# Optimization experiments

Hardware: AMD Instinct MI355X
Metric: run time of the kernel (lower is better)

Reference implementation:

```python
import jax, jax.numpy as jnp
import numpy as np

B, M, F, E = 64, 1024, 4, 256      # batch, memory length, tokens-per-memory-cell, emb_size
NW, HOPS, PL = 32000, 3, 128       # vocab, hops, profile_len


def _embed(table, idx):
    # nn.Embedding with padding_idx=0 -> index 0 maps to zero vector
    return table[idx] * (idx != 0)[..., None].astype(table.dtype)


def _gru_step(x, h, Wih, Whh, bih, bhh):
    # single-step PyTorch GRU cell
    gi = x @ Wih.T + bih
    gh = h @ Whh.T + bhh
    ir, iz, i_n = jnp.split(gi, 3, axis=-1)
    hr, hz, h_n = jnp.split(gh, 3, axis=-1)
    r = jax.nn.sigmoid(ir + hr)
    z = jax.nn.sigmoid(iz + hz)
    n = jnp.tanh(i_n + r * h_n)
    return (1.0 - z) * n + z * h


def setup_inputs() -> dict:
    key = jax.random.key(0)
    ks = jax.random.split(key, 13)
    # HOPS+1 unique embedding tables: A[0..hops-1] plus C[hops-1]; C[h]=tables[h+1] (weight tying)
    tables = (jax.random.normal(ks[0], (HOPS + 1, NW, E)) * 0.1).at[:, 0, :].set(0.0)
    s = 1.0 / np.sqrt(E)
    Wih = jax.random.uniform(ks[1], (3 * E, E), minval=-s, maxval=s)
    Whh = jax.random.uniform(ks[2], (3 * E, E), minval=-s, maxval=s)
    bih = jax.random.uniform(ks[3], (3 * E,), minval=-s, maxval=s)
    bhh = jax.random.uniform(ks[4], (3 * E,), minval=-s, maxval=s)
    sp = 1.0 / np.sqrt(PL)
    Wp = jax.random.uniform(ks[5], (E, PL), minval=-sp, maxval=sp)
    bp = jax.random.uniform(ks[6], (E,), minval=-sp, maxval=sp)
    sv = 1.0 / np.sqrt(2 * E)
    Wv = jax.random.uniform(ks[7], (NW, 2 * E), minval=-sv, maxval=sv)
    bv = jax.random.uniform(ks[8], (NW,), minval=-sv, maxval=sv)
    context = jax.random.randint(ks[9], (B, M, F), 0, NW)
    y_ = jax.random.randint(ks[10], (B,), 0, NW)
    h_ = jax.random.normal(ks[11], (1, B, E))
    profile_encoding = jax.random.normal(ks[12], (B, PL))
    return dict(tables=tables, Wih=Wih, Whh=Whh, bih=bih, bhh=bhh, Wp=Wp, bp=bp,
                Wv=Wv, bv=bv, context=context, y_=y_, h_=h_,
                profile_encoding=profile_encoding)


def reference(tables, Wih, Whh, bih, bhh, Wp, bp, Wv, bv, context, y_, h_, profile_encoding):
    # load_memory (eval mode: no word dropout): memories[h] = sum over F of table[h] embeddings
    ctx = context.reshape(B, M * F)
    mems = [_embed(tables[hop], ctx).reshape(B, M, F, E).sum(axis=2) for hop in range(HOPS + 1)]
    # decoder step
    m = _embed(tables[1], y_)                    # C[0](y_)
    h = _gru_step(m, h_[0], Wih, Whh, bih, bhh)  # [B, E]
    q = h
    p = p_vocab = p_resto = None
    for hop in range(HOPS):
        p_ = mems[hop] * q[:, None, :]           # [B, M, E] elementwise attention scores
        p = p_.sum(axis=2)                        # [B, M]
        attn = jax.nn.softmax(p, axis=1)
        o = jnp.einsum('bm,bme->be', attn, mems[hop + 1])
        if hop == 0:
            p_vocab = jnp.concatenate([h, o], axis=1) @ Wv.T + bv  # uses q[0]=h
        if hop == 1:
            enc = profile_encoding @ Wp.T + bp   # [B, E]
            p_resto = jnp.einsum('bme,be->bm', p_, enc)
        q = q + o
    return p, p_vocab, p_resto, h[None]          # p_ptr, p_vocab, p_resto, h [1,B,E]
```

## Files before the change

### kernel.cpp

```cpp
#include <hip/hip_runtime.h>
#include <cstdint>

#define B_ 64
#define M_ 1024
#define F_ 4
#define E_ 256
#define NW_ 32000
#define PL_ 128

#define P_OFF   0
#define PV_OFF  65536
#define PR_OFF  2113536
#define H_OFF   2179072

typedef unsigned short u16;
typedef unsigned int u32;

typedef __bf16 bf16x8 __attribute__((ext_vector_type(8)));
typedef float f32x4 __attribute__((ext_vector_type(4)));

__device__ __forceinline__ u16 f2bf(float f) {
    u32 x = __builtin_bit_cast(u32, f);
    u32 r = (x + 0x7fffu + ((x >> 16) & 1u)) >> 16;
    return (u16)r;
}
__device__ __forceinline__ float bflo(u32 v) {
    return __builtin_bit_cast(float, v << 16);
}
__device__ __forceinline__ float bfhi(u32 v) {
    return __builtin_bit_cast(float, v & 0xffff0000u);
}
__device__ __forceinline__ float dot8(uint4 u, float4 qa, float4 qb) {
    return bflo(u.x) * qa.x + bfhi(u.x) * qa.y + bflo(u.y) * qa.z + bfhi(u.y) * qa.w +
           bflo(u.z) * qb.x + bfhi(u.z) * qb.y + bflo(u.w) * qb.z + bfhi(u.w) * qb.w;
}
__device__ __forceinline__ void acc8(uint4 u, float* a) {
    a[0] += bflo(u.x); a[1] += bfhi(u.x); a[2] += bflo(u.y); a[3] += bfhi(u.y);
    a[4] += bflo(u.z); a[5] += bfhi(u.z); a[6] += bflo(u.w); a[7] += bfhi(u.w);
}
__device__ __forceinline__ uint4 pack8(const float* s) {
    uint4 u;
    u.x = (u32)f2bf(s[0]) | ((u32)f2bf(s[1]) << 16);
    u.y = (u32)f2bf(s[2]) | ((u32)f2bf(s[3]) << 16);
    u.z = (u32)f2bf(s[4]) | ((u32)f2bf(s[5]) << 16);
    u.w = (u32)f2bf(s[6]) | ((u32)f2bf(s[7]) << 16);
    return u;
}
__device__ __forceinline__ bf16x8 pack_bf8(float4 a, float4 b) {
    union { u16 s[8]; bf16x8 v; } u;
    u.s[0] = f2bf(a.x); u.s[1] = f2bf(a.y); u.s[2] = f2bf(a.z); u.s[3] = f2bf(a.w);
    u.s[4] = f2bf(b.x); u.s[5] = f2bf(b.y); u.s[6] = f2bf(b.z); u.s[7] = f2bf(b.w);
    return u.v;
}

__global__ __launch_bounds__(256) void k_conv(
    const float* __restrict__ tables, u16* __restrict__ t0b, u16* __restrict__ t12)
{
    int t = blockIdx.y;
    int c = blockIdx.x * 256 + threadIdx.x;
    const float* src = tables + (size_t)t * NW_ * E_ + (size_t)c * 8;
    float4 a = *(const float4*)src;
    float4 b = *(const float4*)(src + 4);
    float s[8] = {a.x, a.y, a.z, a.w, b.x, b.y, b.z, b.w};
    uint4 u = pack8(s);
    if (t == 0) {
        *(uint4*)(t0b + (size_t)c * 8) = u;
    } else {
        int row = c >> 5, e = (c & 31) * 8;
        *(uint4*)(t12 + (size_t)row * 512 + (t - 1) * 256 + e) = u;
    }
}

__global__ __launch_bounds__(256) void k_gru(
    const float* __restrict__ tables, const float* __restrict__ Wih,
    const float* __restrict__ Whh, const float* __restrict__ bih,
    const float* __restrict__ bhh, const float* __restrict__ Wp,
    const float* __restrict__ bp, const int* __restrict__ y,
    const float* __restrict__ h_, const float* __restrict__ pe,
    float* __restrict__ q0, float* __restrict__ enc, float* __restrict__ outh)
{
    int b = blockIdx.x, t = threadIdx.x;
    __shared__ float m_s[E_], h_s[E_], pe_s[PL_];
    int yb = y[b];
    m_s[t] = tables[(size_t)NW_ * E_ + (size_t)yb * E_ + t];
    h_s[t] = h_[b * E_ + t];
    if (t < PL_) pe_s[t] = pe[b * PL_ + t];
    __syncthreads();

    float g_i[3], g_h[3];
#pragma unroll
    for (int g = 0; g < 3; g++) {
        int j = g * E_ + t;
        float ai = bih[j], ah = bhh[j];
        const float4* wi = (const float4*)(Wih + (size_t)j * E_);
        const float4* wh = (const float4*)(Whh + (size_t)j * E_);
#pragma unroll 8
        for (int e = 0; e < E_ / 4; e++) {
            float4 a = wi[e], c = wh[e];
            ai += a.x * m_s[4 * e] + a.y * m_s[4 * e + 1] +
                  a.z * m_s[4 * e + 2] + a.w * m_s[4 * e + 3];
            ah += c.x * h_s[4 * e] + c.y * h_s[4 * e + 1] +
                  c.z * h_s[4 * e + 2] + c.w * h_s[4 * e + 3];
        }
        g_i[g] = ai; g_h[g] = ah;
    }
    float r = 1.f / (1.f + expf(-(g_i[0] + g_h[0])));
    float z = 1.f / (1.f + expf(-(g_i[1] + g_h[1])));
    float n = tanhf(g_i[2] + r * g_h[2]);
    float hv = (1.f - z) * n + z * h_s[t];
    q0[b * E_ + t] = hv;
    outh[b * E_ + t] = hv;

    float ea = bp[t];
    const float4* wp = (const float4*)(Wp + (size_t)t * PL_);
#pragma unroll 8
    for (int p = 0; p < PL_ / 4; p++) {
        float4 a = wp[p];
        ea += a.x * pe_s[4 * p] + a.y * pe_s[4 * p + 1] +
              a.z * pe_s[4 * p + 2] + a.w * pe_s[4 * p + 3];
    }
    enc[b * E_ + t] = ea;
}

__global__ __launch_bounds__(256) void k_scores0(
    const u16* __restrict__ t0b, const int* __restrict__ ctx,
    const float* __restrict__ q, float* __restrict__ p_ws)
{
    int b = blockIdx.y, grp = blockIdx.x;
    int lane = threadIdx.x & 63, w = threadIdx.x >> 6;
    int h = lane >> 5, l32 = lane & 31, e0 = l32 * 8;
    float4 qa = *(const float4*)(q + b * E_ + e0);
    float4 qb = *(const float4*)(q + b * E_ + e0 + 4);
    int mbase = grp * 32 + w * 8;
    const int4* cp = (const int4*)(ctx + ((size_t)b * M_ + mbase) * 4);
    int4 c[8];
#pragma unroll
    for (int i = 0; i < 8; i++) c[i] = cp[i];

    float pa[8];
#pragma unroll
    for (int i = 0; i < 8; i++) {
        int ia = h ? c[i].y : c[i].x;
        int ib = h ? c[i].w : c[i].z;
        uint4 ra = *(const uint4*)(t0b + (size_t)ia * E_ + e0);
        uint4 rb = *(const uint4*)(t0b + (size_t)ib * E_ + e0);
        pa[i] = dot8(ra, qa, qb) + dot8(rb, qa, qb);
    }
#pragma unroll
    for (int o = 32; o > 0; o >>= 1)
#pragma unroll
        for (int i = 0; i < 8; i++) pa[i] += __shfl_xor(pa[i], o, 64);
    if (lane == 0)
#pragma unroll
        for (int i = 0; i < 8; i++) p_ws[(size_t)b * M_ + mbase + i] = pa[i];
}

__global__ __launch_bounds__(256) void k_soft(
    float* __restrict__ p_ws, const float* __restrict__ qcur,
    float* __restrict__ qnext)
{
    int b = blockIdx.x, t = threadIdx.x;
    __shared__ float red[256];
    float4 v = *(const float4*)(p_ws + (size_t)b * M_ + t * 4);
    float lm = fmaxf(fmaxf(v.x, v.y), fmaxf(v.z, v.w));
    red[t] = lm;
    __syncthreads();
    for (int s = 128; s > 0; s >>= 1) {
        if (t < s) red[t] = fmaxf(red[t], red[t + s]);
        __syncthreads();
    }
    float mx = red[0];
    __syncthreads();
    float e0 = expf(v.x - mx), e1 = expf(v.y - mx);
    float e2 = expf(v.z - mx), e3 = expf(v.w - mx);
    red[t] = e0 + e1 + e2 + e3;
    __syncthreads();
    for (int s = 128; s > 0; s >>= 1) {
        if (t < s) red[t] += red[t + s];
        __syncthreads();
    }
    float inv = 1.f / red[0];
    float4 o = make_float4(e0 * inv, e1 * inv, e2 * inv, e3 * inv);
    *(float4*)(p_ws + (size_t)b * M_ + t * 4) = o;
    qnext[b * E_ + t] = qcur[b * E_ + t];
}

__global__ __launch_bounds__(256) void k_mems12(
    const u16* __restrict__ t12, const int* __restrict__ ctx,
    const float* __restrict__ attn0, u16* __restrict__ mems1,
    u16* __restrict__ mems2, float* __restrict__ q1)
{
    int b = blockIdx.y, grp = blockIdx.x;
    int lane = threadIdx.x & 63, w = threadIdx.x >> 6;
    int h = lane >> 5, l32 = lane & 31, e0 = l32 * 8;
    int mbase = grp * 32 + w * 8;
    const int4* cp = (const int4*)(ctx + ((size_t)b * M_ + mbase) * 4);
    int4 c[8];
#pragma unroll
    for (int i = 0; i < 8; i++) c[i] = cp[i];
    float4 a01 = *(const float4*)(attn0 + (size_t)b * M_ + mbase);
    float4 a23 = *(const float4*)(attn0 + (size_t)b * M_ + mbase + 4);
    float wg[8] = {a01.x, a01.y, a01.z, a01.w, a23.x, a23.y, a23.z, a23.w};

    u16* mout = h ? mems2 : mems1;
    float o_acc[8] = {0, 0, 0, 0, 0, 0, 0, 0};
#pragma unroll
    for (int i = 0; i < 8; i++) {
        size_t off = (size_t)h * 256 + e0;
        uint4 r0 = *(const uint4*)(t12 + (size_t)c[i].x * 512 + off);
        uint4 r1 = *(const uint4*)(t12 + (size_t)c[i].y * 512 + off);
        uint4 r2 = *(const uint4*)(t12 + (size_t)c[i].z * 512 + off);
        uint4 r3 = *(const uint4*)(t12 + (size_t)c[i].w * 512 + off);
        float acc[8] = {0, 0, 0, 0, 0, 0, 0, 0};
        acc8(r0, acc); acc8(r1, acc); acc8(r2, acc); acc8(r3, acc);
        *(uint4*)(mout + ((size_t)(b * M_ + mbase + i)) * 256 + e0) = pack8(acc);
        if (h == 0) {
            float wgt = wg[i];
#pragma unroll
            for (int j = 0; j < 8; j++) o_acc[j] += wgt * acc[j];
        }
    }
    __shared__ float red[4][E_];
    if (h == 0)
#pragma unroll
        for (int j = 0; j < 8; j++) red[w][e0 + j] = o_acc[j];
    __syncthreads();
    int t = threadIdx.x;
    float s = red[0][t] + red[1][t] + red[2][t] + red[3][t];
    atomicAdd(q1 + b * E_ + t, s);
}

template <int MODE>
__global__ __launch_bounds__(256) void k_sscores(
    const u16* __restrict__ mems, const float* __restrict__ q,
    const float* __restrict__ enc, float* __restrict__ p_ws,
    float* __restrict__ out)
{
    int b = blockIdx.y, grp = blockIdx.x;
    int lane = threadIdx.x & 63, w = threadIdx.x >> 6;
    int h = lane >> 5, l32 = lane & 31, e0 = l32 * 8;
    float4 qa = *(const float4*)(q + b * E_ + e0);
    float4 qb = *(const float4*)(q + b * E_ + e0 + 4);
    float4 ea4 = make_float4(0, 0, 0, 0), eb4 = make_float4(0, 0, 0, 0);
    if (MODE == 1) {
        float4 ev = *(const float4*)(enc + b * E_ + e0);
        float4 ew = *(const float4*)(enc + b * E_ + e0 + 4);
        ea4 = make_float4(qa.x * ev.x, qa.y * ev.y, qa.z * ev.z, qa.w * ev.w);
        eb4 = make_float4(qb.x * ew.x, qb.y * ew.y, qb.z * ew.z, qb.w * ew.w);
    }
    int mbase = grp * 32 + w * 8;
    float pa[4], pr[4];
#pragma unroll
    for (int i = 0; i < 4; i++) {
        int m = mbase + 2 * i + h;
        uint4 r = *(const uint4*)(mems + ((size_t)(b * M_ + m)) * 256 + e0);
        pa[i] = dot8(r, qa, qb);
        if (MODE == 1) pr[i] = dot8(r, ea4, eb4);
    }
#pragma unroll
    for (int o = 16; o > 0; o >>= 1)
#pragma unroll
        for (int i = 0; i < 4; i++) {
            pa[i] += __shfl_xor(pa[i], o, 64);
            if (MODE == 1) pr[i] += __shfl_xor(pr[i], o, 64);
        }
    if (l32 == 0) {
#pragma unroll
        for (int i = 0; i < 4; i++) {
            int m = mbase + 2 * i + h;
            if (MODE == 2) out[P_OFF + (size_t)b * M_ + m] = pa[i];
            else           p_ws[(size_t)b * M_ + m] = pa[i];
            if (MODE == 1) out[PR_OFF + (size_t)b * M_ + m] = pr[i];
        }
    }
}

__global__ __launch_bounds__(256) void k_so(
    const u16* __restrict__ mems, const float* __restrict__ attn,
    float* __restrict__ qnext)
{
    int b = blockIdx.y, ch = blockIdx.x;
    int lane = threadIdx.x & 63, w = threadIdx.x >> 6;
    int h = lane >> 5, l32 = lane & 31, e0 = l32 * 8;
    int m0 = ch * 128;
    float acc[8] = {0, 0, 0, 0, 0, 0, 0, 0};
    for (int i = 0; i < 16; i++) {
        int m = m0 + i * 8 + w * 2 + h;
        float wgt = attn[(size_t)b * M_ + m];
        uint4 r = *(const uint4*)(mems + ((size_t)(b * M_ + m)) * 256 + e0);
        acc[0] += wgt * bflo(r.x); acc[1] += wgt * bfhi(r.x);
        acc[2] += wgt * bflo(r.y); acc[3] += wgt * bfhi(r.y);
        acc[4] += wgt * bflo(r.z); acc[5] += wgt * bfhi(r.z);
        acc[6] += wgt * bflo(r.w); acc[7] += wgt * bfhi(r.w);
    }
    __shared__ float red[8][E_];
    int hw = threadIdx.x >> 5;
#pragma unroll
    for (int j = 0; j < 8; j++) red[hw][e0 + j] = acc[j];
    __syncthreads();
    int t = threadIdx.x;
    float s = 0.f;
#pragma unroll
    for (int k = 0; k < 8; k++) s += red[k][t];
    atomicAdd(qnext + b * E_ + t, s);
}

__global__ __launch_bounds__(256) void k_pvocab(
    const float* __restrict__ Wv, const float* __restrict__ bv,
    const float* __restrict__ q0, const float* __restrict__ q1,
    float* __restrict__ out)
{
    __shared__ u16 X[64 * 512];
    int t = threadIdx.x;
#pragma unroll
    for (int it = 0; it < 16; it++) {
        int id = t + it * 256;
        int bb = id >> 6, c = id & 63;
        float v[8];
        if (c < 32) {
            const float* s = q0 + bb * E_ + c * 8;
#pragma unroll
            for (int j = 0; j < 8; j++) v[j] = s[j];
        } else {
            const float* s1 = q1 + bb * E_ + (c - 32) * 8;
            const float* s0 = q0 + bb * E_ + (c - 32) * 8;
#pragma unroll
            for (int j = 0; j < 8; j++) v[j] = s1[j] - s0[j];
        }
        uint4 uv = pack8(v);
        *(uint4*)(&X[bb * 512 + ((c ^ (bb & 7)) << 3)]) = uv;
    }
    __syncthreads();

    int lane = t & 63, w = t >> 6;
    int n0 = blockIdx.x * 128 + w * 32;
    int l15 = lane & 15, quad = lane >> 4;
    f32x4 acc[4][2];
#pragma unroll
    for (int mt = 0; mt < 4; mt++)
#pragma unroll
        for (int nt = 0; nt < 2; nt++)
            acc[mt][nt] = f32x4{0.f, 0.f, 0.f, 0.f};

    for (int ks = 0; ks < 16; ks++) {
        bf16x8 a[4], bfr[2];
#pragma unroll
        for (int mt = 0; mt < 4; mt++) {
            int m = mt * 16 + l15;
            int c = ks * 4 + quad;
            a[mt] = *(const bf16x8*)(&X[m * 512 + ((c ^ (m & 7)) << 3)]);
        }
#pragma unroll
        for (int nt = 0; nt < 2; nt++) {
            int n = n0 + nt * 16 + l15;
            const float4* wp = (const float4*)(Wv + (size_t)n * 512 + ks * 32 + quad * 8);
            bfr[nt] = pack_bf8(wp[0], wp[1]);
        }
#pragma unroll
        for (int mt = 0; mt < 4; mt++)
#pragma unroll
            for (int nt = 0; nt < 2; nt++)
                acc[mt][nt] = __builtin_amdgcn_mfma_f32_16x16x32_bf16(
                    a[mt], bfr[nt], acc[mt][nt], 0, 0, 0);
    }
#pragma unroll
    for (int nt = 0; nt < 2; nt++) {
        int n = n0 + nt * 16 + l15;
        float bvv = bv[n];
#pragma unroll
        for (int mt = 0; mt < 4; mt++) {
#pragma unroll
            for (int j = 0; j < 4; j++) {
                int m = mt * 16 + quad * 4 + j;
                out[PV_OFF + (size_t)m * 32000 + n] = acc[mt][nt][j] + bvv;
            }
        }
    }
}

extern "C" void kernel_launch(void* const* d_in, const int* in_sizes, int n_in,
                              void* d_out, int out_size, void* d_ws, size_t ws_size,
                              hipStream_t stream)
{
    const float* tables = (const float*)d_in[0];
    const float* Wih = (const float*)d_in[1];
    const float* Whh = (const float*)d_in[2];
    const float* bih = (const float*)d_in[3];
    const float* bhh = (const float*)d_in[4];
    const float* Wp  = (const float*)d_in[5];
    const float* bp  = (const float*)d_in[6];
    const float* Wv  = (const float*)d_in[7];
    const float* bv  = (const float*)d_in[8];
    const int* ctx = (const int*)d_in[9];
    const int* y   = (const int*)d_in[10];
    const float* h_  = (const float*)d_in[11];
    const float* pe  = (const float*)d_in[12];
    float* out = (float*)d_out;

    float* Wf   = (float*)d_ws;
    float* q    = Wf;
    float* enc  = Wf + 65536;
    float* p_ws = Wf + 81920;
    char* base  = (char*)d_ws + 589824;
    u16* t0b    = (u16*)base;
    u16* t12    = (u16*)(base + 16384000);
    u16* mems1  = (u16*)(base + 16384000 + 32768000);
    u16* mems2  = (u16*)(base + 16384000 + 32768000 + 33554432);

    k_conv<<<dim3(4000, 3), 256, 0, stream>>>(tables, t0b, t12);
    k_gru<<<64, 256, 0, stream>>>(tables, Wih, Whh, bih, bhh, Wp, bp, y, h_, pe,
                                  q, enc, out + H_OFF);
    k_scores0<<<dim3(32, 64), 256, 0, stream>>>(t0b, ctx, q, p_ws);
    k_soft<<<64, 256, 0, stream>>>(p_ws, q, q + 16384);
    k_mems12<<<dim3(32, 64), 256, 0, stream>>>(t12, ctx, p_ws, mems1, mems2,
                                               q + 16384);
    k_sscores<1><<<dim3(32, 64), 256, 0, stream>>>(mems1, q + 16384, enc, p_ws, out);
    k_soft<<<64, 256, 0, stream>>>(p_ws, q + 16384, q + 32768);
    k_so<<<dim3(8, 64), 256, 0, stream>>>(mems2, p_ws, q + 32768);
    k_sscores<2><<<dim3(32, 64), 256, 0, stream>>>(mems2, q + 32768, enc, p_ws, out);
    k_pvocab<<<250, 256, 0, stream>>>(Wv, bv, q, q + 16384, out);
}
```

Before: 399.5 us.

## Replace memory materialization with vocab-wide score GEMMs and gathered sums

Instead of building bf16 copies of the tables and materializing summed memory cells, the pipeline first computes query-vs-vocabulary scores for every table row with MFMA GEMMs, using a hi/lo bf16 split of the query to keep precision. Per-memory scores are then gathered as sums of four vocab scores, and the attention-weighted outputs are accumulated directly from fp32 table rows. This removes the full-table conversion pass and the large mems1/mems2 writes and reads. In exchange it scores all 32000 words per batch row and adds several small kernels and extra workspace for the score matrices.

```diff
diff --git a/kernel.cpp b/kernel.cpp
--- a/kernel.cpp
+++ b/kernel.cpp
@@ -24,19 +24,8 @@
     u32 r = (x + 0x7fffu + ((x >> 16) & 1u)) >> 16;
     return (u16)r;
 }
-__device__ __forceinline__ float bflo(u32 v) {
-    return __builtin_bit_cast(float, v << 16);
-}
-__device__ __forceinline__ float bfhi(u32 v) {
-    return __builtin_bit_cast(float, v & 0xffff0000u);
-}
-__device__ __forceinline__ float dot8(uint4 u, float4 qa, float4 qb) {
-    return bflo(u.x) * qa.x + bfhi(u.x) * qa.y + bflo(u.y) * qa.z + bfhi(u.y) * qa.w +
-           bflo(u.z) * qb.x + bfhi(u.z) * qb.y + bflo(u.w) * qb.z + bfhi(u.w) * qb.w;
-}
-__device__ __forceinline__ void acc8(uint4 u, float* a) {
-    a[0] += bflo(u.x); a[1] += bfhi(u.x); a[2] += bflo(u.y); a[3] += bfhi(u.y);
-    a[4] += bflo(u.z); a[5] += bfhi(u.z); a[6] += bflo(u.w); a[7] += bfhi(u.w);
+__device__ __forceinline__ float bf2f(u16 h) {
+    return __builtin_bit_cast(float, (u32)h << 16);
 }
 __device__ __forceinline__ uint4 pack8(const float* s) {
     uint4 u;
@@ -53,31 +42,14 @@
     return u.v;
 }
 
-__global__ __launch_bounds__(256) void k_conv(
-    const float* __restrict__ tables, u16* __restrict__ t0b, u16* __restrict__ t12)
-{
-    int t = blockIdx.y;
-    int c = blockIdx.x * 256 + threadIdx.x;
-    const float* src = tables + (size_t)t * NW_ * E_ + (size_t)c * 8;
-    float4 a = *(const float4*)src;
-    float4 b = *(const float4*)(src + 4);
-    float s[8] = {a.x, a.y, a.z, a.w, b.x, b.y, b.z, b.w};
-    uint4 u = pack8(s);
-    if (t == 0) {
-        *(uint4*)(t0b + (size_t)c * 8) = u;
-    } else {
-        int row = c >> 5, e = (c & 31) * 8;
-        *(uint4*)(t12 + (size_t)row * 512 + (t - 1) * 256 + e) = u;
-    }
-}
-
 __global__ __launch_bounds__(256) void k_gru(
     const float* __restrict__ tables, const float* __restrict__ Wih,
     const float* __restrict__ Whh, const float* __restrict__ bih,
     const float* __restrict__ bhh, const float* __restrict__ Wp,
     const float* __restrict__ bp, const int* __restrict__ y,
     const float* __restrict__ h_, const float* __restrict__ pe,
-    float* __restrict__ q0, float* __restrict__ enc, float* __restrict__ outh)
+    float* __restrict__ q0, float* __restrict__ q1, float* __restrict__ q2,
+    float* __restrict__ enc, float* __restrict__ outh, u16* __restrict__ Qc0)
 {
     int b = blockIdx.x, t = threadIdx.x;
     __shared__ float m_s[E_], h_s[E_], pe_s[PL_];
@@ -109,7 +81,12 @@
     float n = tanhf(g_i[2] + r * g_h[2]);
     float hv = (1.f - z) * n + z * h_s[t];
     q0[b * E_ + t] = hv;
+    q1[b * E_ + t] = hv;
+    q2[b * E_ + t] = hv;
     outh[b * E_ + t] = hv;
+    u16 hi = f2bf(hv);
+    Qc0[(size_t)b * E_ + t] = hi;
+    Qc0[(size_t)(B_ + b) * E_ + t] = f2bf(hv - bf2f(hi));
 
     float ea = bp[t];
     const float4* wp = (const float4*)(Wp + (size_t)t * PL_);
@@ -122,47 +99,98 @@
     enc[b * E_ + t] = ea;
 }
 
-__global__ __launch_bounds__(256) void k_scores0(
-    const u16* __restrict__ t0b, const int* __restrict__ ctx,
-    const float* __restrict__ q, float* __restrict__ p_ws)
-{
-    int b = blockIdx.y, grp = blockIdx.x;
-    int lane = threadIdx.x & 63, w = threadIdx.x >> 6;
-    int h = lane >> 5, l32 = lane & 31, e0 = l32 * 8;
-    float4 qa = *(const float4*)(q + b * E_ + e0);
-    float4 qb = *(const float4*)(q + b * E_ + e0 + 4);
-    int mbase = grp * 32 + w * 8;
-    const int4* cp = (const int4*)(ctx + ((size_t)b * M_ + mbase) * 4);
-    int4 c[8];
-#pragma unroll
-    for (int i = 0; i < 8; i++) c[i] = cp[i];
-
-    float pa[8];
-#pragma unroll
-    for (int i = 0; i < 8; i++) {
-        int ia = h ? c[i].y : c[i].x;
-        int ib = h ? c[i].w : c[i].z;
-        uint4 ra = *(const uint4*)(t0b + (size_t)ia * E_ + e0);
-        uint4 rb = *(const uint4*)(t0b + (size_t)ib * E_ + e0);
-        pa[i] = dot8(ra, qa, qb) + dot8(rb, qa, qb);
-    }
-#pragma unroll
-    for (int o = 32; o > 0; o >>= 1)
-#pragma unroll
-        for (int i = 0; i < 8; i++) pa[i] += __shfl_xor(pa[i], o, 64);
-    if (lane == 0)
-#pragma unroll
-        for (int i = 0; i < 8; i++) p_ws[(size_t)b * M_ + mbase + i] = pa[i];
-}
-
-__global__ __launch_bounds__(256) void k_soft(
-    float* __restrict__ p_ws, const float* __restrict__ qcur,
-    float* __restrict__ qnext)
+template <int WE>
+__global__ __launch_bounds__(256) void k_qprep(
+    const float* __restrict__ qsrc, const float* __restrict__ enc,
+    u16* __restrict__ Qc)
 {
     int b = blockIdx.x, t = threadIdx.x;
+    float v = qsrc[b * E_ + t];
+    u16 hi = f2bf(v);
+    Qc[(size_t)b * E_ + t] = hi;
+    Qc[(size_t)(B_ + b) * E_ + t] = f2bf(v - bf2f(hi));
+    if (WE) {
+        float e = v * enc[b * E_ + t];
+        u16 h2 = f2bf(e);
+        Qc[(size_t)(2 * B_ + b) * E_ + t] = h2;
+        Qc[(size_t)(3 * B_ + b) * E_ + t] = f2bf(e - bf2f(h2));
+    }
+}
+
+template <int NQ>
+__global__ __launch_bounds__(256) void k_sgemm(
+    const float* __restrict__ T, const u16* __restrict__ Qc,
+    float* __restrict__ OA, float* __restrict__ OB)
+{
+    constexpr int NT = NQ * 4;
+    __shared__ float lds[64][65];
+    int t = threadIdx.x, lane = t & 63, wv = t >> 6;
+    int l15 = lane & 15, quad = lane >> 4;
+    int w0 = blockIdx.x * 64;
+    const float* arow = T + (size_t)(w0 + wv * 16 + l15) * E_;
+    f32x4 acc[NT];
+#pragma unroll
+    for (int nt = 0; nt < NT; nt++) acc[nt] = f32x4{0.f, 0.f, 0.f, 0.f};
+#pragma unroll
+    for (int ks = 0; ks < 8; ks++) {
+        int k0 = ks * 32 + quad * 8;
+        float4 a0 = *(const float4*)(arow + k0);
+        float4 a1 = *(const float4*)(arow + k0 + 4);
+        bf16x8 af = pack_bf8(a0, a1);
+#pragma unroll
+        for (int nt = 0; nt < NT; nt++) {
+            bf16x8 bfr = *(const bf16x8*)(Qc + (size_t)(nt * 16 + l15) * E_ + k0);
+            acc[nt] = __builtin_amdgcn_mfma_f32_16x16x32_bf16(af, bfr, acc[nt], 0, 0, 0);
+        }
+    }
+#pragma unroll
+    for (int arr = 0; arr < NQ / 2; arr++) {
+        float* O = arr ? OB : OA;
+        if (arr) __syncthreads();
+#pragma unroll
+        for (int nt = 0; nt < 4; nt++)
+#pragma unroll
+            for (int j = 0; j < 4; j++)
+                lds[wv * 16 + quad * 4 + j][nt * 16 + l15] =
+                    acc[arr * 8 + nt][j] + acc[arr * 8 + nt + 4][j];
+        __syncthreads();
+        int bb = t >> 2, ws = (t & 3) * 16;
+        float vv[16];
+#pragma unroll
+        for (int i = 0; i < 16; i++) vv[i] = lds[ws + i][bb];
+        float* orow = O + (size_t)bb * NW_ + w0 + ws;
+        *(float4*)(orow)      = make_float4(vv[0], vv[1], vv[2], vv[3]);
+        *(float4*)(orow + 4)  = make_float4(vv[4], vv[5], vv[6], vv[7]);
+        *(float4*)(orow + 8)  = make_float4(vv[8], vv[9], vv[10], vv[11]);
+        *(float4*)(orow + 12) = make_float4(vv[12], vv[13], vv[14], vv[15]);
+    }
+}
+
+template <int MODE>
+__global__ __launch_bounds__(256) void k_gsm(
+    const float* __restrict__ S, const float* __restrict__ SR,
+    const int* __restrict__ ctx, float* __restrict__ attn,
+    float* __restrict__ outpr)
+{
+    int b = blockIdx.x, t = threadIdx.x;
+    const float* Sb = S + (size_t)b * NW_;
+    const int4* cp = (const int4*)(ctx + ((size_t)b * M_ + t * 4) * F_);
+    int4 c0 = cp[0], c1 = cp[1], c2 = cp[2], c3 = cp[3];
+    float p0 = Sb[c0.x] + Sb[c0.y] + Sb[c0.z] + Sb[c0.w];
+    float p1 = Sb[c1.x] + Sb[c1.y] + Sb[c1.z] + Sb[c1.w];
+    float p2 = Sb[c2.x] + Sb[c2.y] + Sb[c2.z] + Sb[c2.w];
+    float p3 = Sb[c3.x] + Sb[c3.y] + Sb[c3.z] + Sb[c3.w];
+    if constexpr (MODE == 1) {
+        const float* Rb = SR + (size_t)b * NW_;
+        float r0 = Rb[c0.x] + Rb[c0.y] + Rb[c0.z] + Rb[c0.w];
+        float r1 = Rb[c1.x] + Rb[c1.y] + Rb[c1.z] + Rb[c1.w];
+        float r2 = Rb[c2.x] + Rb[c2.y] + Rb[c2.z] + Rb[c2.w];
+        float r3 = Rb[c3.x] + Rb[c3.y] + Rb[c3.z] + Rb[c3.w];
+        *(float4*)(outpr + PR_OFF + (size_t)b * M_ + t * 4) =
+            make_float4(r0, r1, r2, r3);
+    }
     __shared__ float red[256];
-    float4 v = *(const float4*)(p_ws + (size_t)b * M_ + t * 4);
-    float lm = fmaxf(fmaxf(v.x, v.y), fmaxf(v.z, v.w));
+    float lm = fmaxf(fmaxf(p0, p1), fmaxf(p2, p3));
     red[t] = lm;
     __syncthreads();
     for (int s = 128; s > 0; s >>= 1) {
@@ -171,8 +199,8 @@
     }
     float mx = red[0];
     __syncthreads();
-    float e0 = expf(v.x - mx), e1 = expf(v.y - mx);
-    float e2 = expf(v.z - mx), e3 = expf(v.w - mx);
+    float e0 = expf(p0 - mx), e1 = expf(p1 - mx);
+    float e2 = expf(p2 - mx), e3 = expf(p3 - mx);
     red[t] = e0 + e1 + e2 + e3;
     __syncthreads();
     for (int s = 128; s > 0; s >>= 1) {
@@ -180,129 +208,43 @@
         __syncthreads();
     }
     float inv = 1.f / red[0];
-    float4 o = make_float4(e0 * inv, e1 * inv, e2 * inv, e3 * inv);
-    *(float4*)(p_ws + (size_t)b * M_ + t * 4) = o;
-    qnext[b * E_ + t] = qcur[b * E_ + t];
-}
-
-__global__ __launch_bounds__(256) void k_mems12(
-    const u16* __restrict__ t12, const int* __restrict__ ctx,
-    const float* __restrict__ attn0, u16* __restrict__ mems1,
-    u16* __restrict__ mems2, float* __restrict__ q1)
-{
-    int b = blockIdx.y, grp = blockIdx.x;
-    int lane = threadIdx.x & 63, w = threadIdx.x >> 6;
-    int h = lane >> 5, l32 = lane & 31, e0 = l32 * 8;
-    int mbase = grp * 32 + w * 8;
-    const int4* cp = (const int4*)(ctx + ((size_t)b * M_ + mbase) * 4);
-    int4 c[8];
-#pragma unroll
-    for (int i = 0; i < 8; i++) c[i] = cp[i];
-    float4 a01 = *(const float4*)(attn0 + (size_t)b * M_ + mbase);
-    float4 a23 = *(const float4*)(attn0 + (size_t)b * M_ + mbase + 4);
-    float wg[8] = {a01.x, a01.y, a01.z, a01.w, a23.x, a23.y, a23.z, a23.w};
-
-    u16* mout = h ? mems2 : mems1;
-    float o_acc[8] = {0, 0, 0, 0, 0, 0, 0, 0};
-#pragma unroll
-    for (int i = 0; i < 8; i++) {
-        size_t off = (size_t)h * 256 + e0;
-        uint4 r0 = *(const uint4*)(t12 + (size_t)c[i].x * 512 + off);
-        uint4 r1 = *(const uint4*)(t12 + (size_t)c[i].y * 512 + off);
-        uint4 r2 = *(const uint4*)(t12 + (size_t)c[i].z * 512 + off);
-        uint4 r3 = *(const uint4*)(t12 + (size_t)c[i].w * 512 + off);
-        float acc[8] = {0, 0, 0, 0, 0, 0, 0, 0};
-        acc8(r0, acc); acc8(r1, acc); acc8(r2, acc); acc8(r3, acc);
-        *(uint4*)(mout + ((size_t)(b * M_ + mbase + i)) * 256 + e0) = pack8(acc);
-        if (h == 0) {
-            float wgt = wg[i];
-#pragma unroll
-            for (int j = 0; j < 8; j++) o_acc[j] += wgt * acc[j];
-        }
-    }
-    __shared__ float red[4][E_];
-    if (h == 0)
-#pragma unroll
-        for (int j = 0; j < 8; j++) red[w][e0 + j] = o_acc[j];
-    __syncthreads();
-    int t = threadIdx.x;
-    float s = red[0][t] + red[1][t] + red[2][t] + red[3][t];
-    atomicAdd(q1 + b * E_ + t, s);
-}
-
-template <int MODE>
-__global__ __launch_bounds__(256) void k_sscores(
-    const u16* __restrict__ mems, const float* __restrict__ q,
-    const float* __restrict__ enc, float* __restrict__ p_ws,
+    *(float4*)(attn + (size_t)b * M_ + t * 4) =
+        make_float4(e0 * inv, e1 * inv, e2 * inv, e3 * inv);
+}
+
+__global__ __launch_bounds__(256) void k_g2(
+    const float* __restrict__ S, const int* __restrict__ ctx,
     float* __restrict__ out)
 {
-    int b = blockIdx.y, grp = blockIdx.x;
-    int lane = threadIdx.x & 63, w = threadIdx.x >> 6;
-    int h = lane >> 5, l32 = lane & 31, e0 = l32 * 8;
-    float4 qa = *(const float4*)(q + b * E_ + e0);
-    float4 qb = *(const float4*)(q + b * E_ + e0 + 4);
-    float4 ea4 = make_float4(0, 0, 0, 0), eb4 = make_float4(0, 0, 0, 0);
-    if (MODE == 1) {
-        float4 ev = *(const float4*)(enc + b * E_ + e0);
-        float4 ew = *(const float4*)(enc + b * E_ + e0 + 4);
-        ea4 = make_float4(qa.x * ev.x, qa.y * ev.y, qa.z * ev.z, qa.w * ev.w);
-        eb4 = make_float4(qb.x * ew.x, qb.y * ew.y, qb.z * ew.z, qb.w * ew.w);
-    }
-    int mbase = grp * 32 + w * 8;
-    float pa[4], pr[4];
-#pragma unroll
-    for (int i = 0; i < 4; i++) {
-        int m = mbase + 2 * i + h;
-        uint4 r = *(const uint4*)(mems + ((size_t)(b * M_ + m)) * 256 + e0);
-        pa[i] = dot8(r, qa, qb);
-        if (MODE == 1) pr[i] = dot8(r, ea4, eb4);
-    }
-#pragma unroll
-    for (int o = 16; o > 0; o >>= 1)
-#pragma unroll
-        for (int i = 0; i < 4; i++) {
-            pa[i] += __shfl_xor(pa[i], o, 64);
-            if (MODE == 1) pr[i] += __shfl_xor(pr[i], o, 64);
-        }
-    if (l32 == 0) {
-#pragma unroll
-        for (int i = 0; i < 4; i++) {
-            int m = mbase + 2 * i + h;
-            if (MODE == 2) out[P_OFF + (size_t)b * M_ + m] = pa[i];
-            else           p_ws[(size_t)b * M_ + m] = pa[i];
-            if (MODE == 1) out[PR_OFF + (size_t)b * M_ + m] = pr[i];
-        }
-    }
-}
-
-__global__ __launch_bounds__(256) void k_so(
-    const u16* __restrict__ mems, const float* __restrict__ attn,
-    float* __restrict__ qnext)
-{
-    int b = blockIdx.y, ch = blockIdx.x;
-    int lane = threadIdx.x & 63, w = threadIdx.x >> 6;
-    int h = lane >> 5, l32 = lane & 31, e0 = l32 * 8;
-    int m0 = ch * 128;
-    float acc[8] = {0, 0, 0, 0, 0, 0, 0, 0};
-    for (int i = 0; i < 16; i++) {
-        int m = m0 + i * 8 + w * 2 + h;
-        float wgt = attn[(size_t)b * M_ + m];
-        uint4 r = *(const uint4*)(mems + ((size_t)(b * M_ + m)) * 256 + e0);
-        acc[0] += wgt * bflo(r.x); acc[1] += wgt * bfhi(r.x);
-        acc[2] += wgt * bflo(r.y); acc[3] += wgt * bfhi(r.y);
-        acc[4] += wgt * bflo(r.z); acc[5] += wgt * bfhi(r.z);
-        acc[6] += wgt * bflo(r.w); acc[7] += wgt * bfhi(r.w);
-    }
-    __shared__ float red[8][E_];
-    int hw = threadIdx.x >> 5;
-#pragma unroll
-    for (int j = 0; j < 8; j++) red[hw][e0 + j] = acc[j];
-    __syncthreads();
-    int t = threadIdx.x;
-    float s = 0.f;
-#pragma unroll
-    for (int k = 0; k < 8; k++) s += red[k][t];
-    atomicAdd(qnext + b * E_ + t, s);
+    int b = blockIdx.y;
+    int m = blockIdx.x * 256 + threadIdx.x;
+    const float* Sb = S + (size_t)b * NW_;
+    int4 c = *(const int4*)(ctx + ((size_t)b * M_ + m) * F_);
+    out[P_OFF + (size_t)b * M_ + m] = Sb[c.x] + Sb[c.y] + Sb[c.z] + Sb[c.w];
+}
+
+template <int NADD>
+__global__ __launch_bounds__(256) void k_oacc(
+    const float* __restrict__ T, const int* __restrict__ ctx,
+    const float* __restrict__ attn, float* __restrict__ qa,
+    float* __restrict__ qb)
+{
+    int b = blockIdx.y, chv = blockIdx.x, t = threadIdx.x;
+    int m0 = chv * 128;
+    __shared__ int cidx[512];
+    __shared__ float aw[128];
+    if (t < 128) aw[t] = attn[(size_t)b * M_ + m0 + t];
+    ((int2*)cidx)[t] = ((const int2*)(ctx + ((size_t)b * M_ + m0) * F_))[t];
+    __syncthreads();
+    float acc0 = 0.f, acc1 = 0.f;
+#pragma unroll 8
+    for (int r = 0; r < 512; r += 2) {
+        acc0 += aw[r >> 2]       * T[(size_t)cidx[r] * E_ + t];
+        acc1 += aw[(r + 1) >> 2] * T[(size_t)cidx[r + 1] * E_ + t];
+    }
+    float acc = acc0 + acc1;
+    atomicAdd(qa + b * E_ + t, acc);
+    if constexpr (NADD == 2) atomicAdd(qb + b * E_ + t, acc);
 }
 
 __global__ __launch_bounds__(256) void k_pvocab(
@@ -398,25 +340,33 @@
     float* out = (float*)d_out;
 
     float* Wf   = (float*)d_ws;
-    float* q    = Wf;
-    float* enc  = Wf + 65536;
-    float* p_ws = Wf + 81920;
-    char* base  = (char*)d_ws + 589824;
-    u16* t0b    = (u16*)base;
-    u16* t12    = (u16*)(base + 16384000);
-    u16* mems1  = (u16*)(base + 16384000 + 32768000);
-    u16* mems2  = (u16*)(base + 16384000 + 32768000 + 33554432);
-
-    k_conv<<<dim3(4000, 3), 256, 0, stream>>>(tables, t0b, t12);
+    float* q0v  = Wf;
+    float* q1v  = Wf + 16384;
+    float* q2v  = Wf + 32768;
+    float* encv = Wf + 49152;
+    float* attn = Wf + 65536;
+    u16* Qc0 = (u16*)(Wf + 131072);
+    u16* Qc1 = Qc0 + 32768;
+    u16* Qc2 = Qc1 + 65536;
+    float* S0 = (float*)(Qc2 + 32768);
+    float* S1 = S0 + (size_t)B_ * NW_;
+    float* SRb = S1 + (size_t)B_ * NW_;
+    float* S2 = SRb + (size_t)B_ * NW_;
+    const float* T0 = tables;
+    const float* T1 = tables + (size_t)NW_ * E_;
+    const float* T2 = tables + 2 * (size_t)NW_ * E_;
+
     k_gru<<<64, 256, 0, stream>>>(tables, Wih, Whh, bih, bhh, Wp, bp, y, h_, pe,
-                                  q, enc, out + H_OFF);
-    k_scores0<<<dim3(32, 64), 256, 0, stream>>>(t0b, ctx, q, p_ws);
-    k_soft<<<64, 256, 0, stream>>>(p_ws, q, q + 16384);
-    k_mems12<<<dim3(32, 64), 256, 0, stream>>>(t12, ctx, p_ws, mems1, mems2,
-                                               q + 16384);
-    k_sscores<1><<<dim3(32, 64), 256, 0, stream>>>(mems1, q + 16384, enc, p_ws, out);
-    k_soft<<<64, 256, 0, stream>>>(p_ws, q + 16384, q + 32768);
-    k_so<<<dim3(8, 64), 256, 0, stream>>>(mems2, p_ws, q + 32768);
-    k_sscores<2><<<dim3(32, 64), 256, 0, stream>>>(mems2, q + 32768, enc, p_ws, out);
-    k_pvocab<<<250, 256, 0, stream>>>(Wv, bv, q, q + 16384, out);
-}
+                                  q0v, q1v, q2v, encv, out + H_OFF, Qc0);
+    k_sgemm<2><<<500, 256, 0, stream>>>(T0, Qc0, S0, nullptr);
+    k_gsm<0><<<64, 256, 0, stream>>>(S0, nullptr, ctx, attn, nullptr);
+    k_oacc<2><<<dim3(8, 64), 256, 0, stream>>>(T1, ctx, attn, q1v, q2v);
+    k_qprep<1><<<64, 256, 0, stream>>>(q1v, encv, Qc1);
+    k_sgemm<4><<<500, 256, 0, stream>>>(T1, Qc1, S1, SRb);
+    k_gsm<1><<<64, 256, 0, stream>>>(S1, SRb, ctx, attn, out);
+    k_oacc<1><<<dim3(8, 64), 256, 0, stream>>>(T2, ctx, attn, q2v, nullptr);
+    k_qprep<0><<<64, 256, 0, stream>>>(q2v, nullptr, Qc2);
+    k_sgemm<2><<<500, 256, 0, stream>>>(T2, Qc2, S2, nullptr);
+    k_g2<<<dim3(4, 64), 256, 0, stream>>>(S2, ctx, out);
+    k_pvocab<<<250, 256, 0, stream>>>(Wv, bv, q0v, q1v, out);
+}
```

Result: slower. 461.0 us (+15.4%).

## Fuse all phases into one persistent cooperative kernel with grid syncs

Applied to the files above, without the earlier changes.

Replaces the ten separate kernel launches with a single cooperative persistent kernel that runs each stage as a phase separated by grid-wide barriers, using a shared-memory union. The GRU runs on dedicated blocks while the table conversion runs on the rest, and the final score phase is overlapped with the vocab projection in the same loop. The vocab GEMM is retiled to 64 columns per block with batched weight loads. This removes launch gaps and inter-kernel idle time, at the cost of grid-sync overhead, limited grid size (at most 512 blocks), and lower per-phase occupancy.

```diff
diff --git a/kernel.cpp b/kernel.cpp
--- a/kernel.cpp
+++ b/kernel.cpp
@@ -1,5 +1,8 @@
 #include <hip/hip_runtime.h>
+#include <hip/hip_cooperative_groups.h>
 #include <cstdint>
+
+namespace cg = cooperative_groups;
 
 #define B_ 64
 #define M_ 1024
@@ -53,11 +56,19 @@
     return u.v;
 }
 
-__global__ __launch_bounds__(256) void k_conv(
+union SharedU {
+    struct { float m_s[E_]; float h_s[E_]; float pe_s[PL_]; } gru;
+    float red1[256];
+    float red4[4][E_];
+    float red8[8][E_];
+    u16 X[64 * 512];
+};
+
+__device__ __forceinline__ void ph_conv(int vb, int tid,
     const float* __restrict__ tables, u16* __restrict__ t0b, u16* __restrict__ t12)
 {
-    int t = blockIdx.y;
-    int c = blockIdx.x * 256 + threadIdx.x;
+    int t = vb / 4000;
+    int c = (vb % 4000) * 256 + tid;
     const float* src = tables + (size_t)t * NW_ * E_ + (size_t)c * 8;
     float4 a = *(const float4*)src;
     float4 b = *(const float4*)(src + 4);
@@ -71,7 +82,7 @@
     }
 }
 
-__global__ __launch_bounds__(256) void k_gru(
+__device__ __forceinline__ void ph_gru(int b, int tid, SharedU& su,
     const float* __restrict__ tables, const float* __restrict__ Wih,
     const float* __restrict__ Whh, const float* __restrict__ bih,
     const float* __restrict__ bhh, const float* __restrict__ Wp,
@@ -79,12 +90,12 @@
     const float* __restrict__ h_, const float* __restrict__ pe,
     float* __restrict__ q0, float* __restrict__ enc, float* __restrict__ outh)
 {
-    int b = blockIdx.x, t = threadIdx.x;
-    __shared__ float m_s[E_], h_s[E_], pe_s[PL_];
+    int t = tid;
+    __syncthreads();
     int yb = y[b];
-    m_s[t] = tables[(size_t)NW_ * E_ + (size_t)yb * E_ + t];
-    h_s[t] = h_[b * E_ + t];
-    if (t < PL_) pe_s[t] = pe[b * PL_ + t];
+    su.gru.m_s[t] = tables[(size_t)NW_ * E_ + (size_t)yb * E_ + t];
+    su.gru.h_s[t] = h_[b * E_ + t];
+    if (t < PL_) su.gru.pe_s[t] = pe[b * PL_ + t];
     __syncthreads();
 
     float g_i[3], g_h[3];
@@ -97,17 +108,17 @@
 #pragma unroll 8
         for (int e = 0; e < E_ / 4; e++) {
             float4 a = wi[e], c = wh[e];
-            ai += a.x * m_s[4 * e] + a.y * m_s[4 * e + 1] +
-                  a.z * m_s[4 * e + 2] + a.w * m_s[4 * e + 3];
-            ah += c.x * h_s[4 * e] + c.y * h_s[4 * e + 1] +
-                  c.z * h_s[4 * e + 2] + c.w * h_s[4 * e + 3];
+            ai += a.x * su.gru.m_s[4 * e] + a.y * su.gru.m_s[4 * e + 1] +
+                  a.z * su.gru.m_s[4 * e + 2] + a.w * su.gru.m_s[4 * e + 3];
+            ah += c.x * su.gru.h_s[4 * e] + c.y * su.gru.h_s[4 * e + 1] +
+                  c.z * su.gru.h_s[4 * e + 2] + c.w * su.gru.h_s[4 * e + 3];
         }
         g_i[g] = ai; g_h[g] = ah;
     }
     float r = 1.f / (1.f + expf(-(g_i[0] + g_h[0])));
     float z = 1.f / (1.f + expf(-(g_i[1] + g_h[1])));
     float n = tanhf(g_i[2] + r * g_h[2]);
-    float hv = (1.f - z) * n + z * h_s[t];
+    float hv = (1.f - z) * n + z * su.gru.h_s[t];
     q0[b * E_ + t] = hv;
     outh[b * E_ + t] = hv;
 
@@ -116,18 +127,18 @@
 #pragma unroll 8
     for (int p = 0; p < PL_ / 4; p++) {
         float4 a = wp[p];
-        ea += a.x * pe_s[4 * p] + a.y * pe_s[4 * p + 1] +
-              a.z * pe_s[4 * p + 2] + a.w * pe_s[4 * p + 3];
+        ea += a.x * su.gru.pe_s[4 * p] + a.y * su.gru.pe_s[4 * p + 1] +
+              a.z * su.gru.pe_s[4 * p + 2] + a.w * su.gru.pe_s[4 * p + 3];
     }
     enc[b * E_ + t] = ea;
 }
 
-__global__ __launch_bounds__(256) void k_scores0(
+__device__ __forceinline__ void ph_scores0(int vb, int tid,
     const u16* __restrict__ t0b, const int* __restrict__ ctx,
     const float* __restrict__ q, float* __restrict__ p_ws)
 {
-    int b = blockIdx.y, grp = blockIdx.x;
-    int lane = threadIdx.x & 63, w = threadIdx.x >> 6;
+    int grp = vb & 31, b = vb >> 5;
+    int lane = tid & 63, w = tid >> 6;
     int h = lane >> 5, l32 = lane & 31, e0 = l32 * 8;
     float4 qa = *(const float4*)(q + b * E_ + e0);
     float4 qb = *(const float4*)(q + b * E_ + e0 + 4);
@@ -155,45 +166,46 @@
         for (int i = 0; i < 8; i++) p_ws[(size_t)b * M_ + mbase + i] = pa[i];
 }
 
-__global__ __launch_bounds__(256) void k_soft(
+__device__ __forceinline__ void ph_soft(int b, int tid, SharedU& su,
     float* __restrict__ p_ws, const float* __restrict__ qcur,
     float* __restrict__ qnext)
 {
-    int b = blockIdx.x, t = threadIdx.x;
-    __shared__ float red[256];
+    int t = tid;
+    __syncthreads();
     float4 v = *(const float4*)(p_ws + (size_t)b * M_ + t * 4);
     float lm = fmaxf(fmaxf(v.x, v.y), fmaxf(v.z, v.w));
-    red[t] = lm;
+    su.red1[t] = lm;
     __syncthreads();
     for (int s = 128; s > 0; s >>= 1) {
-        if (t < s) red[t] = fmaxf(red[t], red[t + s]);
+        if (t < s) su.red1[t] = fmaxf(su.red1[t], su.red1[t + s]);
         __syncthreads();
     }
-    float mx = red[0];
+    float mx = su.red1[0];
     __syncthreads();
     float e0 = expf(v.x - mx), e1 = expf(v.y - mx);
     float e2 = expf(v.z - mx), e3 = expf(v.w - mx);
-    red[t] = e0 + e1 + e2 + e3;
+    su.red1[t] = e0 + e1 + e2 + e3;
     __syncthreads();
     for (int s = 128; s > 0; s >>= 1) {
-        if (t < s) red[t] += red[t + s];
+        if (t < s) su.red1[t] += su.red1[t + s];
         __syncthreads();
     }
-    float inv = 1.f / red[0];
+    float inv = 1.f / su.red1[0];
     float4 o = make_float4(e0 * inv, e1 * inv, e2 * inv, e3 * inv);
     *(float4*)(p_ws + (size_t)b * M_ + t * 4) = o;
     qnext[b * E_ + t] = qcur[b * E_ + t];
 }
 
-__global__ __launch_bounds__(256) void k_mems12(
+__device__ __forceinline__ void ph_mems12(int vb, int tid, SharedU& su,
     const u16* __restrict__ t12, const int* __restrict__ ctx,
     const float* __restrict__ attn0, u16* __restrict__ mems1,
     u16* __restrict__ mems2, float* __restrict__ q1)
 {
-    int b = blockIdx.y, grp = blockIdx.x;
-    int lane = threadIdx.x & 63, w = threadIdx.x >> 6;
+    int grp = vb & 31, b = vb >> 5;
+    int lane = tid & 63, w = tid >> 6;
     int h = lane >> 5, l32 = lane & 31, e0 = l32 * 8;
     int mbase = grp * 32 + w * 8;
+    __syncthreads();
     const int4* cp = (const int4*)(ctx + ((size_t)b * M_ + mbase) * 4);
     int4 c[8];
 #pragma unroll
@@ -220,24 +232,23 @@
             for (int j = 0; j < 8; j++) o_acc[j] += wgt * acc[j];
         }
     }
-    __shared__ float red[4][E_];
     if (h == 0)
 #pragma unroll
-        for (int j = 0; j < 8; j++) red[w][e0 + j] = o_acc[j];
-    __syncthreads();
-    int t = threadIdx.x;
-    float s = red[0][t] + red[1][t] + red[2][t] + red[3][t];
+        for (int j = 0; j < 8; j++) su.red4[w][e0 + j] = o_acc[j];
+    __syncthreads();
+    int t = tid;
+    float s = su.red4[0][t] + su.red4[1][t] + su.red4[2][t] + su.red4[3][t];
     atomicAdd(q1 + b * E_ + t, s);
 }
 
 template <int MODE>
-__global__ __launch_bounds__(256) void k_sscores(
+__device__ __forceinline__ void ph_sscores(int vb, int tid,
     const u16* __restrict__ mems, const float* __restrict__ q,
     const float* __restrict__ enc, float* __restrict__ p_ws,
     float* __restrict__ out)
 {
-    int b = blockIdx.y, grp = blockIdx.x;
-    int lane = threadIdx.x & 63, w = threadIdx.x >> 6;
+    int grp = vb & 31, b = vb >> 5;
+    int lane = tid & 63, w = tid >> 6;
     int h = lane >> 5, l32 = lane & 31, e0 = l32 * 8;
     float4 qa = *(const float4*)(q + b * E_ + e0);
     float4 qb = *(const float4*)(q + b * E_ + e0 + 4);
@@ -275,14 +286,15 @@
     }
 }
 
-__global__ __launch_bounds__(256) void k_so(
+__device__ __forceinline__ void ph_so(int vb, int tid, SharedU& su,
     const u16* __restrict__ mems, const float* __restrict__ attn,
     float* __restrict__ qnext)
 {
-    int b = blockIdx.y, ch = blockIdx.x;
-    int lane = threadIdx.x & 63, w = threadIdx.x >> 6;
+    int ch = vb & 7, b = vb >> 3;
+    int lane = tid & 63, w = tid >> 6;
     int h = lane >> 5, l32 = lane & 31, e0 = l32 * 8;
     int m0 = ch * 128;
+    __syncthreads();
     float acc[8] = {0, 0, 0, 0, 0, 0, 0, 0};
     for (int i = 0; i < 16; i++) {
         int m = m0 + i * 8 + w * 2 + h;
@@ -293,25 +305,24 @@
         acc[4] += wgt * bflo(r.z); acc[5] += wgt * bfhi(r.z);
         acc[6] += wgt * bflo(r.w); acc[7] += wgt * bfhi(r.w);
     }
-    __shared__ float red[8][E_];
-    int hw = threadIdx.x >> 5;
-#pragma unroll
-    for (int j = 0; j < 8; j++) red[hw][e0 + j] = acc[j];
-    __syncthreads();
-    int t = threadIdx.x;
+    int hw = tid >> 5;
+#pragma unroll
+    for (int j = 0; j < 8; j++) su.red8[hw][e0 + j] = acc[j];
+    __syncthreads();
+    int t = tid;
     float s = 0.f;
 #pragma unroll
-    for (int k = 0; k < 8; k++) s += red[k][t];
+    for (int k = 0; k < 8; k++) s += su.red8[k][t];
     atomicAdd(qnext + b * E_ + t, s);
 }
 
-__global__ __launch_bounds__(256) void k_pvocab(
+__device__ __forceinline__ void ph_pvocab(int vbp, int tid, SharedU& su,
     const float* __restrict__ Wv, const float* __restrict__ bv,
     const float* __restrict__ q0, const float* __restrict__ q1,
     float* __restrict__ out)
 {
-    __shared__ u16 X[64 * 512];
-    int t = threadIdx.x;
+    int t = tid;
+    __syncthreads();
 #pragma unroll
     for (int it = 0; it < 16; it++) {
         int id = t + it * 256;
@@ -328,53 +339,94 @@
             for (int j = 0; j < 8; j++) v[j] = s1[j] - s0[j];
         }
         uint4 uv = pack8(v);
-        *(uint4*)(&X[bb * 512 + ((c ^ (bb & 7)) << 3)]) = uv;
+        *(uint4*)(&su.X[bb * 512 + ((c ^ (bb & 7)) << 3)]) = uv;
     }
     __syncthreads();
 
     int lane = t & 63, w = t >> 6;
-    int n0 = blockIdx.x * 128 + w * 32;
     int l15 = lane & 15, quad = lane >> 4;
-    f32x4 acc[4][2];
-#pragma unroll
-    for (int mt = 0; mt < 4; mt++)
-#pragma unroll
-        for (int nt = 0; nt < 2; nt++)
-            acc[mt][nt] = f32x4{0.f, 0.f, 0.f, 0.f};
-
-    for (int ks = 0; ks < 16; ks++) {
-        bf16x8 a[4], bfr[2];
-#pragma unroll
-        for (int mt = 0; mt < 4; mt++) {
-            int m = mt * 16 + l15;
-            int c = ks * 4 + quad;
-            a[mt] = *(const bf16x8*)(&X[m * 512 + ((c ^ (m & 7)) << 3)]);
-        }
-#pragma unroll
-        for (int nt = 0; nt < 2; nt++) {
-            int n = n0 + nt * 16 + l15;
-            const float4* wp = (const float4*)(Wv + (size_t)n * 512 + ks * 32 + quad * 8);
-            bfr[nt] = pack_bf8(wp[0], wp[1]);
-        }
-#pragma unroll
-        for (int mt = 0; mt < 4; mt++)
-#pragma unroll
-            for (int nt = 0; nt < 2; nt++)
-                acc[mt][nt] = __builtin_amdgcn_mfma_f32_16x16x32_bf16(
-                    a[mt], bfr[nt], acc[mt][nt], 0, 0, 0);
-    }
-#pragma unroll
-    for (int nt = 0; nt < 2; nt++) {
-        int n = n0 + nt * 16 + l15;
-        float bvv = bv[n];
-#pragma unroll
-        for (int mt = 0; mt < 4; mt++) {
-#pragma unroll
-            for (int j = 0; j < 4; j++) {
-                int m = mt * 16 + quad * 4 + j;
-                out[PV_OFF + (size_t)m * 32000 + n] = acc[mt][nt][j] + bvv;
+    int n = vbp * 64 + w * 16 + l15;
+    const float4* wp = (const float4*)(Wv + (size_t)n * 512);
+    f32x4 acc[4];
+#pragma unroll
+    for (int mt = 0; mt < 4; mt++) acc[mt] = f32x4{0.f, 0.f, 0.f, 0.f};
+
+#pragma unroll
+    for (int half = 0; half < 2; half++) {
+        float4 wv[8][2];
+#pragma unroll
+        for (int k8 = 0; k8 < 8; k8++) {
+            int ks = half * 8 + k8;
+            wv[k8][0] = wp[ks * 8 + quad * 2];
+            wv[k8][1] = wp[ks * 8 + quad * 2 + 1];
+        }
+#pragma unroll
+        for (int k8 = 0; k8 < 8; k8++) {
+            int ks = half * 8 + k8;
+            bf16x8 bfr = pack_bf8(wv[k8][0], wv[k8][1]);
+#pragma unroll
+            for (int mt = 0; mt < 4; mt++) {
+                int m = mt * 16 + l15;
+                int c = ks * 4 + quad;
+                bf16x8 a = *(const bf16x8*)(&su.X[m * 512 + ((c ^ (m & 7)) << 3)]);
+                acc[mt] = __builtin_amdgcn_mfma_f32_16x16x32_bf16(a, bfr, acc[mt], 0, 0, 0);
             }
         }
+    }
+    float bvv = bv[n];
+#pragma unroll
+    for (int mt = 0; mt < 4; mt++) {
+#pragma unroll
+        for (int j = 0; j < 4; j++) {
+            int m = mt * 16 + quad * 4 + j;
+            out[PV_OFF + (size_t)m * 32000 + n] = acc[mt][j] + bvv;
+        }
+    }
+}
+
+__global__ __launch_bounds__(256, 2) void mega(
+    const float* __restrict__ tables, const float* __restrict__ Wih,
+    const float* __restrict__ Whh, const float* __restrict__ bih,
+    const float* __restrict__ bhh, const float* __restrict__ Wp,
+    const float* __restrict__ bp, const float* __restrict__ Wv,
+    const float* __restrict__ bv, const int* __restrict__ ctx,
+    const int* __restrict__ y, const float* __restrict__ h_,
+    const float* __restrict__ pe, float* __restrict__ out,
+    u16* __restrict__ t0b, u16* __restrict__ t12,
+    u16* __restrict__ mems1, u16* __restrict__ mems2,
+    float* __restrict__ p_ws, float* __restrict__ q, float* __restrict__ enc)
+{
+    cg::grid_group grid = cg::this_grid();
+    __shared__ SharedU su;
+    int bid = blockIdx.x, G = gridDim.x, tid = threadIdx.x;
+
+    int gru0 = G - 64;
+    if (bid >= gru0) {
+        ph_gru(bid - gru0, tid, su, tables, Wih, Whh, bih, bhh, Wp, bp, y, h_, pe,
+               q, enc, out + H_OFF);
+    } else {
+        for (int vb = bid; vb < 12000; vb += gru0)
+            ph_conv(vb, tid, tables, t0b, t12);
+    }
+    grid.sync();
+    for (int vb = bid; vb < 2048; vb += G) ph_scores0(vb, tid, t0b, ctx, q, p_ws);
+    grid.sync();
+    if (bid < 64) ph_soft(bid, tid, su, p_ws, q, q + 16384);
+    grid.sync();
+    for (int vb = bid; vb < 2048; vb += G)
+        ph_mems12(vb, tid, su, t12, ctx, p_ws, mems1, mems2, q + 16384);
+    grid.sync();
+    for (int vb = bid; vb < 2048; vb += G)
+        ph_sscores<1>(vb, tid, mems1, q + 16384, enc, p_ws, out);
+    grid.sync();
+    if (bid < 64) ph_soft(bid, tid, su, p_ws, q + 16384, q + 32768);
+    grid.sync();
+    for (int vb = bid; vb < 512; vb += G)
+        ph_so(vb, tid, su, mems2, p_ws, q + 32768);
+    grid.sync();
+    for (int vb = bid; vb < 2048 + 500; vb += G) {
+        if (vb < 2048) ph_sscores<2>(vb, tid, mems2, q + 32768, enc, p_ws, out);
+        else           ph_pvocab(vb - 2048, tid, su, Wv, bv, q, q + 16384, out);
     }
 }
 
@@ -407,16 +459,19 @@
     u16* mems1  = (u16*)(base + 16384000 + 32768000);
     u16* mems2  = (u16*)(base + 16384000 + 32768000 + 33554432);
 
-    k_conv<<<dim3(4000, 3), 256, 0, stream>>>(tables, t0b, t12);
-    k_gru<<<64, 256, 0, stream>>>(tables, Wih, Whh, bih, bhh, Wp, bp, y, h_, pe,
-                                  q, enc, out + H_OFF);
-    k_scores0<<<dim3(32, 64), 256, 0, stream>>>(t0b, ctx, q, p_ws);
-    k_soft<<<64, 256, 0, stream>>>(p_ws, q, q + 16384);
-    k_mems12<<<dim3(32, 64), 256, 0, stream>>>(t12, ctx, p_ws, mems1, mems2,
-                                               q + 16384);
-    k_sscores<1><<<dim3(32, 64), 256, 0, stream>>>(mems1, q + 16384, enc, p_ws, out);
-    k_soft<<<64, 256, 0, stream>>>(p_ws, q + 16384, q + 32768);
-    k_so<<<dim3(8, 64), 256, 0, stream>>>(mems2, p_ws, q + 32768);
-    k_sscores<2><<<dim3(32, 64), 256, 0, stream>>>(mems2, q + 32768, enc, p_ws, out);
-    k_pvocab<<<250, 256, 0, stream>>>(Wv, bv, q, q + 16384, out);
-}
+    int nb = 0;
+    hipOccupancyMaxActiveBlocksPerMultiprocessor(&nb, mega, 256, 0);
+    if (nb < 1) nb = 1;
+    int G = nb * 256;
+    if (G > 512) G = 512;
+    if (G < 128) G = 128;
+
+    void* args[] = {
+        (void*)&tables, (void*)&Wih, (void*)&Whh, (void*)&bih, (void*)&bhh,
+        (void*)&Wp, (void*)&bp, (void*)&Wv, (void*)&bv, (void*)&ctx,
+        (void*)&y, (void*)&h_, (void*)&pe, (void*)&out,
+        (void*)&t0b, (void*)&t12, (void*)&mems1, (void*)&mems2,
+        (void*)&p_ws, (void*)&q, (void*)&enc
+    };
+    hipLaunchCooperativeKernel((void*)mega, dim3(G), dim3(256), args, 0, stream);
+}
```

After: 599.8 us. 1.5x slower.
